# Performance work log

Measured on AMD Instinct MI355X. Metric: run time of the kernel, lower is better.

Reference implementation:

```python
import jax, jax.numpy as jnp
import numpy as np
import math

B_SZ, T_LEN, DIM = 1, 1024, 1024
D_STATE, EXPAND, NUM_SCALES, CONV_K = 16, 2, 3, 4
D_INNER = EXPAND * DIM
EPS_LOG = 1e-38
LN_EPS = 1e-5


def _causal_dwconv(x, w, b):
    # x: (B,T,D), w: (D,1,K) depthwise, b: (D,). torch Conv1d(pad=K-1)[:, :, :T] == left-pad K-1 (causal).
    y = jax.lax.conv_general_dilated(
        jnp.transpose(x, (0, 2, 1)), w, window_strides=(1,),
        padding=[(CONV_K - 1, 0)], dimension_numbers=('NCH', 'OIH', 'NCH'),
        feature_group_count=w.shape[0])
    return jnp.transpose(y, (0, 2, 1)) + b


def _ssm_core(x, cw, cb, xw, dtw, dtb, Dp):
    # x: (B,T,d_inner)
    xc = jax.nn.silu(_causal_dwconv(x, cw, cb))
    proj = xc @ xw.T                               # (B,T,2*d_state)
    B_ssm, C_ssm = proj[..., :D_STATE], proj[..., D_STATE:]
    dt = jax.nn.softplus(B_ssm @ dtw.T + dtb)      # (B,T,d_inner)
    dt = jax.nn.softplus(dt)                       # selective_scan applies softplus a second time (faithful)
    A = -jnp.arange(1, D_STATE + 1, dtype=xc.dtype)  # (d_state,) == -A_init row, same for every d_inner channel
    dA = jnp.exp(dt[..., None] * A)                # (B,T,d_inner,d_state)
    dBx = dt[..., None] * B_ssm[:, :, None, :] * xc[..., None]
    log_dA = jnp.log(jnp.clip(dA, EPS_LOG))
    log_dBx = jnp.log(jnp.clip(dBx, EPS_LOG))
    # parallel_scan_cpu: h = exp(cumsum(log_dA) + logcumsumexp(log_dBx - cumsum(log_dA)))
    a_star = jnp.cumsum(log_dA, axis=1)
    h = jnp.exp(a_star + jax.lax.cumlogsumexp(log_dBx - a_star, axis=1))
    return jnp.einsum('bts,btds->btd', C_ssm, h) + Dp * xc


def _downsample(x, stride):
    if stride == 1:
        return x
    Bb, T, D = x.shape
    Tt = (T // stride) * stride
    return x[:, :Tt].reshape(Bb, Tt // stride, stride, D).mean(2)


def _upsample(x, T_out):
    # F.interpolate(mode='linear', align_corners=False)
    T_in = x.shape[1]
    if T_in == T_out:
        return x
    scale = T_in / T_out
    pos = jnp.clip((jnp.arange(T_out, dtype=jnp.float32) + 0.5) * scale - 0.5, 0.0, T_in - 1)
    lo = jnp.floor(pos).astype(jnp.int32)
    hi = jnp.minimum(lo + 1, T_in - 1)
    w = (pos - lo.astype(pos.dtype))[None, :, None]
    return x[:, lo] * (1.0 - w) + x[:, hi] * w


def _forward(x, in_proj_w, conv_w, conv_b, xproj_w, dtproj_w, dtproj_b,
             D_param, scale_weights, gate_w1, gate_w2, out_proj_w, ln_g, ln_b):
    residual = x
    xz = x @ in_proj_w.T                           # (B,T,2*d_inner)
    x_in, gate = xz[..., :D_INNER], xz[..., D_INNER:]
    outs = []
    for s in range(NUM_SCALES):
        x_s = _downsample(x_in, 2 ** s)
        y_s = _ssm_core(x_s, conv_w[s], conv_b[s], xproj_w[s], dtproj_w[s], dtproj_b[s], D_param[s])
        outs.append(_upsample(y_s, x.shape[1]))
    w = jax.nn.softmax(scale_weights)
    fused = sum(w[s] * outs[s] for s in range(NUM_SCALES))
    ctx = sum(outs) / NUM_SCALES
    gate_ctx = jax.nn.sigmoid(jax.nn.silu(ctx @ gate_w1.T) @ gate_w2.T)
    out = (fused * gate_ctx) * jax.nn.silu(gate)
    out = out @ out_proj_w.T
    y = out + residual
    mu = y.mean(-1, keepdims=True)
    var = ((y - mu) ** 2).mean(-1, keepdims=True)
    return (y - mu) / jnp.sqrt(var + LN_EPS) * ln_g + ln_b


def setup_inputs() -> dict:
    key = jax.random.key(0)
    ks = jax.random.split(key, 12)
    g = lambda k, shp, s: (jax.random.normal(k, shp, jnp.float32) * s)
    return {
        'x': g(ks[0], (B_SZ, T_LEN, DIM), 1.0),
        'in_proj_w': g(ks[1], (2 * D_INNER, DIM), DIM ** -0.5),
        'conv_w': g(ks[2], (NUM_SCALES, D_INNER, 1, CONV_K), CONV_K ** -0.5),
        'conv_b': g(ks[3], (NUM_SCALES, D_INNER), 0.02),
        'xproj_w': g(ks[4], (NUM_SCALES, 2 * D_STATE, D_INNER), D_INNER ** -0.5),
        'dtproj_w': g(ks[5], (NUM_SCALES, D_INNER, D_STATE), D_STATE ** -0.5),
        'dtproj_b': jax.random.uniform(ks[6], (NUM_SCALES, D_INNER), jnp.float32,
                                       math.log(0.001), math.log(0.1)),
        'D_param': jnp.ones((NUM_SCALES, D_INNER), jnp.float32),
        'scale_weights': jnp.ones((NUM_SCALES,), jnp.float32) / NUM_SCALES,
        'gate_w1': g(ks[7], (D_INNER // 2, D_INNER), D_INNER ** -0.5),
        'gate_w2': g(ks[8], (D_INNER, D_INNER // 2), (D_INNER // 2) ** -0.5),
        'out_proj_w': g(ks[9], (DIM, D_INNER), D_INNER ** -0.5),
        'ln_g': jnp.ones((DIM,), jnp.float32),
        'ln_b': jnp.zeros((DIM,), jnp.float32),
    }


def reference(x, in_proj_w, conv_w, conv_b, xproj_w, dtproj_w, dtproj_b,
              D_param, scale_weights, gate_w1, gate_w2, out_proj_w, ln_g, ln_b):
    return _forward(x, in_proj_w, conv_w, conv_b, xproj_w, dtproj_w, dtproj_b,
                    D_param, scale_weights, gate_w1, gate_w2, out_proj_w, ln_g, ln_b)
```

## Files before the change

kernel.cpp:

```cpp
#include <hip/hip_runtime.h>

typedef unsigned short u16;
typedef float floatx4 __attribute__((ext_vector_type(4)));
typedef short shortx8 __attribute__((ext_vector_type(8)));

#define DIN 2048

__device__ __forceinline__ u16 f2bf(float f){
  unsigned u = __float_as_uint(f);
  u = (u + 0x7fffu + ((u>>16)&1u))>>16;
  return (u16)u;
}
__device__ __forceinline__ float sigf(float x){ return 1.f/(1.f+__expf(-x)); }
__device__ __forceinline__ float siluf(float x){ return x*sigf(x); }

#define OFF_WINP  0ull
#define OFF_WG1   8388608ull
#define OFF_WG2   12582912ull
#define OFF_WOP   16777216ull
#define OFF_XB    20971520ull
#define OFF_XIN   23068672ull
#define OFF_SGATE 31457280ull
#define OFF_X1    39845888ull
#define OFF_X2    44040192ull
#define OFF_XC0   46137344ull
#define OFF_XC1   54525952ull
#define OFF_XC2   58720256ull
#define OFF_FUSED 60817408ull
#define OFF_G3O   69206016ull
#define OFF_Y0    75497472ull
#define OFF_Y1    83886080ull
#define OFF_Y2    88080384ull
#define OFF_P0    90177536ull
#define OFF_P1    90308608ull
#define OFF_P2    90374144ull
#define OFF_CTXB  OFF_XC0
#define OFF_T1B   OFF_XC1
#define OFF_PS    OFF_Y0
#define OFF_HINIT OFF_XIN
#define OFF_T1A0  OFF_XIN
#define OFF_T1A1  OFF_X1
#define OFF_YPA0  OFF_Y1
#define OFF_YPA1  (OFF_XC0 + 4194304ull)
#define OFF_DT0   OFF_FUSED
#define OFF_DT1   OFF_G3O
#define OFF_DT2   (OFF_G3O + 4194304ull)

__device__ __forceinline__ void gld_lds16(const void* g, void* l){
  __builtin_amdgcn_global_load_lds((const __attribute__((address_space(1))) unsigned*)g,
                                   (__attribute__((address_space(3))) unsigned*)l, 16, 0, 0);
}

__global__ __launch_bounds__(256) void cvt_kernel(
    const float* __restrict__ s0, u16* __restrict__ d0,
    const float* __restrict__ s1, u16* __restrict__ d1,
    const float* __restrict__ s2, u16* __restrict__ d2,
    const float* __restrict__ s3, u16* __restrict__ d3,
    const float* __restrict__ s4, u16* __restrict__ d4)
{
  int i = (blockIdx.x*256 + threadIdx.x)*4;
  const float* s; u16* d;
  if      (i <  4194304){ s=s0; d=d0; }
  else if (i <  6291456){ s=s1; d=d1; i -=  4194304; }
  else if (i <  8388608){ s=s2; d=d2; i -=  6291456; }
  else if (i < 10485760){ s=s3; d=d3; i -=  8388608; }
  else                  { s=s4; d=d4; i -= 10485760; }
  const float4 v = *(const float4*)(s + i);
  ushort4 o; o.x = f2bf(v.x); o.y = f2bf(v.y); o.z = f2bf(v.z); o.w = f2bf(v.w);
  *(ushort4*)(d + i) = o;
}

template<int MODE, int BM>
__global__ __launch_bounds__(256) void gemm_bt(
    const u16* __restrict__ A, const u16* __restrict__ B,
    int N, int K, int Ks,
    float* __restrict__ out_f, float* __restrict__ out_f2, u16* __restrict__ out_b,
    const float* __restrict__ ex0f, const float* __restrict__ ex1f,
    float* __restrict__ ex0, float* __restrict__ ex1)
{
  constexpr int NI = BM/32;
  constexpr int IP = BM/64;
  __shared__ u16 smA[2][BM*32];
  __shared__ u16 smB[2][BM*32];
  const int tid  = threadIdx.x;
  const int m0   = blockIdx.y * BM;
  const int n0   = blockIdx.x * BM;
  const int wv   = tid >> 6;
  const int lane = tid & 63;
  const int mw   = (wv >> 1) * (BM/2);
  const int nw   = (wv & 1) * (BM/2);
  const int quad = lane >> 4;
  const int l16  = lane & 15;
  const int srow = tid >> 2;
  const int scol = (tid & 3) * 8;

  floatx4 acc[NI][NI];
#pragma unroll
  for (int i=0;i<NI;i++)
#pragma unroll
    for (int j=0;j<NI;j++) acc[i][j] = (floatx4)0.f;

  const int kStart = blockIdx.z * Ks;
  const int kEnd   = kStart + Ks;

  auto stage = [&](int buf, int k0){
#pragma unroll
    for (int p=0;p<IP;p++){
      gld_lds16(A + (size_t)(m0 + p*64 + srow)*K + k0 + scol, &smA[buf][p*2048 + wv*512]);
      gld_lds16(B + (size_t)(n0 + p*64 + srow)*K + k0 + scol, &smB[buf][p*2048 + wv*512]);
    }
  };

  stage(0, kStart);
  int cur = 0;
  for (int k0 = kStart; k0 < kEnd; k0 += 32) {
    __syncthreads();
    if (k0 + 32 < kEnd) stage(cur^1, k0+32);
    shortx8 af[NI], bfr[NI];
#pragma unroll
    for (int i=0;i<NI;i++){
      af[i]  = *(const shortx8*)&smA[cur][(mw + i*16 + l16)*32 + quad*8];
      bfr[i] = *(const shortx8*)&smB[cur][(nw + i*16 + l16)*32 + quad*8];
    }
#pragma unroll
    for (int i=0;i<NI;i++)
#pragma unroll
      for (int j=0;j<NI;j++)
        acc[i][j] = __builtin_amdgcn_mfma_f32_16x16x32_bf16(af[i], bfr[j], acc[i][j], 0, 0, 0);
    cur ^= 1;
  }

#pragma unroll
  for (int i=0;i<NI;i++){
    const int mb = m0 + mw + i*16 + quad*4;
#pragma unroll
    for (int j=0;j<NI;j++){
      const int n = n0 + nw + j*16 + l16;
      const floatx4 v4 = acc[i][j];
      if (MODE == 0){
        if (n < 2048){
#pragma unroll
          for (int r=0;r<4;r++) out_f[(size_t)(mb+r)*2048 + n] = v4[r];
          ex0[(size_t)(mb>>1)*2048 + n]       = 0.5f*(v4[0]+v4[1]);
          ex0[(size_t)((mb>>1)+1)*2048 + n]   = 0.5f*(v4[2]+v4[3]);
          ex1[(size_t)(mb>>2)*2048 + n]       = 0.25f*(v4[0]+v4[1]+v4[2]+v4[3]);
        } else {
#pragma unroll
          for (int r=0;r<4;r++) out_f2[(size_t)(mb+r)*2048 + (n-2048)] = siluf(v4[r]);
        }
      } else if (MODE == 2){
#pragma unroll
        for (int r=0;r<4;r++){
          const size_t idx = (size_t)(mb+r)*N + n;
          out_b[idx] = f2bf(sigf(v4[r]) * ex0f[idx] * ex1f[idx]);
        }
      } else {
        float* dst = blockIdx.z ? out_f2 : out_f;
#pragma unroll
        for (int r=0;r<4;r++) dst[(size_t)(mb+r)*N + n] = v4[r];
      }
    }
  }
}

__global__ __launch_bounds__(256) void g2_epi(const float* __restrict__ a,
    const float* __restrict__ b, u16* __restrict__ o){
  const int i = (blockIdx.x*256 + threadIdx.x)*4;
  const float4 va = *(const float4*)(a+i);
  const float4 vb = *(const float4*)(b+i);
  ushort4 r;
  r.x = f2bf(siluf(va.x+vb.x)); r.y = f2bf(siluf(va.y+vb.y));
  r.z = f2bf(siluf(va.z+vb.z)); r.w = f2bf(siluf(va.w+vb.w));
  *(ushort4*)(o+i) = r;
}

__global__ __launch_bounds__(256) void conv_kernel(const float* __restrict__ xin,
    const float* __restrict__ x1, const float* __restrict__ x2,
    const float* __restrict__ cw, const float* __restrict__ cb,
    float* __restrict__ xc0, float* __restrict__ xc1, float* __restrict__ xc2){
  const int idx = blockIdx.x*256 + threadIdx.x;
  const float* xs; float* xc; int s, local;
  if (idx < 1024*DIN)              { s=0; local=idx;             xs=xin; xc=xc0; }
  else if (idx < (1024+512)*DIN)   { s=1; local=idx-1024*DIN;    xs=x1;  xc=xc1; }
  else                             { s=2; local=idx-1536*DIN;    xs=x2;  xc=xc2; }
  const int t = local >> 11, d = local & 2047;
  const float* w = cw + ((size_t)(s*DIN) + d)*4;
  float acc = cb[s*DIN + d];
#pragma unroll
  for (int j=0;j<4;j++){
    const int tt = t - 3 + j;
    if (tt >= 0) acc += w[j] * xs[(size_t)tt*DIN + d];
  }
  xc[local] = siluf(acc);
}

__global__ __launch_bounds__(256) void xproj_kernel(const float* __restrict__ xc0,
    const float* __restrict__ xc1, const float* __restrict__ xc2,
    const float* __restrict__ xw,
    float* __restrict__ p0, float* __restrict__ p1, float* __restrict__ p2){
  __shared__ float srow[DIN];
  const int b = blockIdx.x;
  const float* xc; float* proj; int s, t;
  if (b < 1024)      { s=0; t=b;       xc=xc0; proj=p0; }
  else if (b < 1536) { s=1; t=b-1024;  xc=xc1; proj=p1; }
  else               { s=2; t=b-1536;  xc=xc2; proj=p2; }
  const float* xr = xc + (size_t)t*DIN;
  const int tid = threadIdx.x;
#pragma unroll
  for (int q=0;q<2;q++){
    const int k = (q*256 + tid)*4;
    *(float4*)&srow[k] = *(const float4*)&xr[k];
  }
  __syncthreads();
  const int i = tid >> 3;
  const int j = tid & 7;
  const float* w = xw + ((size_t)s*32 + i)*DIN;
  float acc = 0.f;
#pragma unroll 8
  for (int c=0;c<256;c++){
    const int k = j + 8*c;
    acc += srow[k]*w[k];
  }
  acc += __shfl_xor(acc,1); acc += __shfl_xor(acc,2); acc += __shfl_xor(acc,4);
  if (j == 0) proj[t*32 + i] = acc;
}

__global__ __launch_bounds__(128) void scan_p1(
    const float* __restrict__ xc0, const float* __restrict__ xc1, const float* __restrict__ xc2,
    const float* __restrict__ p0,  const float* __restrict__ p1,  const float* __restrict__ p2,
    const float* __restrict__ dtw, const float* __restrict__ dtb,
    float* __restrict__ dt0, float* __restrict__ dt1, float* __restrict__ dt2,
    float2* __restrict__ PS)
{
  __shared__ float sproj[32*32];
  int b = blockIdx.x;
  const float *xc, *proj; float* dto; int base, s;
  if (b < 512)      { xc=xc0; proj=p0; dto=dt0; base=0;  s=0; }
  else if (b < 768) { b-=512; xc=xc1; proj=p1; dto=dt1; base=32; s=1; }
  else              { b-=768; xc=xc2; proj=p2; dto=dt2; base=48; s=2; }
  const int chunk = b >> 4;
  const int tid   = threadIdx.x;
  const int d     = (b & 15)*128 + tid;
  const int t0    = chunk*32;
  {
    const int k = tid*8;
    *(float4*)&sproj[k]   = *(const float4*)&proj[t0*32 + k];
    *(float4*)&sproj[k+4] = *(const float4*)&proj[t0*32 + k + 4];
  }
  __syncthreads();

  float wreg[16];
  const float* wr = dtw + ((size_t)(s*DIN) + d)*16;
#pragma unroll
  for (int n=0;n<16;n++) wreg[n] = wr[n];
  const float bias = dtb[s*DIN + d];

  float H[16];
#pragma unroll
  for (int n=0;n<16;n++) H[n] = 0.f;
  float S = 0.f;
  const float* xcp = xc + (size_t)t0*DIN + d;
  float* dtp = dto + (size_t)t0*DIN + d;
  for (int tt=0; tt<32; tt++){
    const float xcv = xcp[(size_t)tt*DIN];
    const float* Bp = &sproj[tt*32];
    float z = bias;
#pragma unroll
    for (int n=0;n<16;n++) z += Bp[n]*wreg[n];
    z = fminf(z, 60.f);
    const float E     = __expf(z);
    const float denom = 2.f + E;
    const float e     = __builtin_amdgcn_rcpf(denom);
    const float dtv   = __logf(denom);
    dtp[(size_t)tt*DIN] = dtv;
    S += dtv;
    const float c = dtv*xcv;
    float ep = e;
#pragma unroll
    for (int n=0;n<16;n++){
      const float dA  = fmaxf(ep, 1e-38f);
      const float dBx = fmaxf(c*Bp[n], 1e-38f);
      H[n] = dA*H[n] + dBx;
      ep *= e;
    }
  }
  const float q = __expf(-S);
  float qp = q;
  float2* o = PS + ((size_t)(base+chunk)*2048 + d)*16;
#pragma unroll
  for (int n=0;n<16;n++){ float2 v; v.x = qp; v.y = H[n]; o[n] = v; qp *= q; }
}

__global__ __launch_bounds__(256) void scan_combine(const float2* __restrict__ PS,
                                                    float* __restrict__ Hinit){
  int id = blockIdx.x*256 + threadIdx.x;
  int base, C;
  if (id < 32768)      { base=0;  C=32; }
  else if (id < 65536) { id-=32768; base=32; C=16; }
  else                 { id-=65536; base=48; C=8;  }
  const size_t off = (size_t)base*32768 + id;
  const float2* ps = PS + off;
  float* hi = Hinit + off;
  float H = 0.f;
  for (int c=0;c<C;c++){
    hi[(size_t)c*32768] = H;
    const float2 v = ps[(size_t)c*32768];
    H = v.x*H + v.y;
  }
}

__global__ __launch_bounds__(128) void scan_p2(
    const float* __restrict__ xc0, const float* __restrict__ xc1, const float* __restrict__ xc2,
    const float* __restrict__ p0,  const float* __restrict__ p1,  const float* __restrict__ p2,
    const float* __restrict__ dt0, const float* __restrict__ dt1, const float* __restrict__ dt2,
    const float* __restrict__ Hinit, const float* __restrict__ Dp_all,
    float* __restrict__ y0, float* __restrict__ y1, float* __restrict__ y2)
{
  __shared__ float sproj[32*32];
  int b = blockIdx.x;
  const float *xc, *proj, *dti; float* y; int base, s;
  if (b < 512)      { xc=xc0; proj=p0; dti=dt0; y=y0; base=0;  s=0; }
  else if (b < 768) { b-=512; xc=xc1; proj=p1; dti=dt1; y=y1; base=32; s=1; }
  else              { b-=768; xc=xc2; proj=p2; dti=dt2; y=y2; base=48; s=2; }
  const int chunk = b >> 4;
  const int tid   = threadIdx.x;
  const int d     = (b & 15)*128 + tid;
  const int t0    = chunk*32;
  {
    const int k = tid*8;
    *(float4*)&sproj[k]   = *(const float4*)&proj[t0*32 + k];
    *(float4*)&sproj[k+4] = *(const float4*)&proj[t0*32 + k + 4];
  }
  __syncthreads();

  float H[16];
  const float* hi = Hinit + ((size_t)(base+chunk)*2048 + d)*16;
#pragma unroll
  for (int n=0;n<16;n++) H[n] = hi[n];
  const float Dv = Dp_all[s*DIN + d];
  const float* xcp = xc + (size_t)t0*DIN + d;
  const float* dtp = dti + (size_t)t0*DIN + d;
  float* yp = y + (size_t)t0*DIN + d;
  for (int tt=0; tt<32; tt++){
    const float xcv = xcp[(size_t)tt*DIN];
    const float dtv = dtp[(size_t)tt*DIN];
    const float* Bp = &sproj[tt*32];
    const float e = __expf(-dtv);
    const float c = dtv*xcv;
    float ep = e;
    float pacc = 0.f;
#pragma unroll
    for (int n=0;n<16;n++){
      const float dA  = fmaxf(ep, 1e-38f);
      const float dBx = fmaxf(c*Bp[n], 1e-38f);
      H[n] = dA*H[n] + dBx;
      pacc += Bp[16+n]*H[n];
      ep *= e;
    }
    yp[(size_t)tt*DIN] = pacc + Dv*xcv;
  }
}

__device__ __forceinline__ float ups_read(const float* __restrict__ ys, int Tin, int t, int d){
  const float scale = (float)Tin * (1.f/1024.f);
  float pos = ((float)t + 0.5f)*scale - 0.5f;
  pos = fminf(fmaxf(pos, 0.f), (float)(Tin-1));
  const int lo = (int)floorf(pos);
  const float w = pos - (float)lo;
  const int hi = min(lo+1, Tin-1);
  return ys[(size_t)lo*DIN + d]*(1.f-w) + ys[(size_t)hi*DIN + d]*w;
}

__global__ __launch_bounds__(256) void fuse_kernel(const float* __restrict__ y0,
    const float* __restrict__ y1, const float* __restrict__ y2,
    const float* __restrict__ sw, u16* __restrict__ ctxb, float* __restrict__ fused){
  const int idx = blockIdx.x*256 + threadIdx.x;
  const int t = idx >> 11, d = idx & 2047;
  const float w0r = sw[0], w1r = sw[1], w2r = sw[2];
  const float mx = fmaxf(w0r, fmaxf(w1r, w2r));
  float e0 = __expf(w0r-mx), e1 = __expf(w1r-mx), e2 = __expf(w2r-mx);
  const float inv = 1.f/(e0+e1+e2);
  e0 *= inv; e1 *= inv; e2 *= inv;
  const float o0 = y0[idx];
  const float o1 = ups_read(y1, 512, t, d);
  const float o2 = ups_read(y2, 256, t, d);
  fused[idx] = e0*o0 + e1*o1 + e2*o2;
  ctxb[idx]  = f2bf((o0+o1+o2)*(1.f/3.f));
}

__global__ __launch_bounds__(256) void ln_kernel(const float* __restrict__ ya,
    const float* __restrict__ yb, const float* __restrict__ xr,
    const float* __restrict__ g, const float* __restrict__ b, float* __restrict__ out){
  __shared__ float red[4];
  const int t = blockIdx.x;
  const size_t ro = (size_t)t*1024;
  float v[4];
  float s = 0.f;
#pragma unroll
  for (int i=0;i<4;i++){
    const int c = threadIdx.x + i*256;
    v[i] = ya[ro+c] + yb[ro+c] + xr[ro+c];
    s += v[i];
  }
  s += __shfl_xor(s,1); s += __shfl_xor(s,2); s += __shfl_xor(s,4);
  s += __shfl_xor(s,8); s += __shfl_xor(s,16); s += __shfl_xor(s,32);
  if ((threadIdx.x & 63) == 0) red[threadIdx.x>>6] = s;
  __syncthreads();
  const float mu = (red[0]+red[1]+red[2]+red[3]) * (1.f/1024.f);
  __syncthreads();
  float q = 0.f;
#pragma unroll
  for (int i=0;i<4;i++){ const float dd = v[i]-mu; q += dd*dd; }
  q += __shfl_xor(q,1); q += __shfl_xor(q,2); q += __shfl_xor(q,4);
  q += __shfl_xor(q,8); q += __shfl_xor(q,16); q += __shfl_xor(q,32);
  if ((threadIdx.x & 63) == 0) red[threadIdx.x>>6] = q;
  __syncthreads();
  const float rstd = rsqrtf((red[0]+red[1]+red[2]+red[3]) * (1.f/1024.f) + 1e-5f);
#pragma unroll
  for (int i=0;i<4;i++){
    const int c = threadIdx.x + i*256;
    out[ro + c] = (v[i]-mu)*rstd*g[c] + b[c];
  }
}

extern "C" void kernel_launch(void* const* d_in, const int* in_sizes, int n_in,
                              void* d_out, int out_size, void* d_ws, size_t ws_size,
                              hipStream_t stream) {
  const float* x     = (const float*)d_in[0];
  const float* inpw  = (const float*)d_in[1];
  const float* convw = (const float*)d_in[2];
  const float* convb = (const float*)d_in[3];
  const float* xpw   = (const float*)d_in[4];
  const float* dtw   = (const float*)d_in[5];
  const float* dtb   = (const float*)d_in[6];
  const float* Dp    = (const float*)d_in[7];
  const float* sw    = (const float*)d_in[8];
  const float* gw1   = (const float*)d_in[9];
  const float* gw2   = (const float*)d_in[10];
  const float* opw   = (const float*)d_in[11];
  const float* lng   = (const float*)d_in[12];
  const float* lnb   = (const float*)d_in[13];
  float* out = (float*)d_out;

  char* ws = (char*)d_ws;
  u16*    wInp  = (u16*)   (ws + OFF_WINP);
  u16*    wG1   = (u16*)   (ws + OFF_WG1);
  u16*    wG2   = (u16*)   (ws + OFF_WG2);
  u16*    wOp   = (u16*)   (ws + OFF_WOP);
  u16*    xb    = (u16*)   (ws + OFF_XB);
  float*  xin   = (float*) (ws + OFF_XIN);
  float*  sgate = (float*) (ws + OFF_SGATE);
  float*  x1    = (float*) (ws + OFF_X1);
  float*  x2    = (float*) (ws + OFF_X2);
  float*  xc0   = (float*) (ws + OFF_XC0);
  float*  xc1   = (float*) (ws + OFF_XC1);
  float*  xc2   = (float*) (ws + OFF_XC2);
  float*  dt0   = (float*) (ws + OFF_DT0);
  float*  dt1   = (float*) (ws + OFF_DT1);
  float*  dt2   = (float*) (ws + OFF_DT2);
  float*  y0    = (float*) (ws + OFF_Y0);
  float*  y1    = (float*) (ws + OFF_Y1);
  float*  y2    = (float*) (ws + OFF_Y2);
  float*  p0    = (float*) (ws + OFF_P0);
  float*  p1    = (float*) (ws + OFF_P1);
  float*  p2    = (float*) (ws + OFF_P2);
  float2* PS    = (float2*)(ws + OFF_PS);
  float*  Hinit = (float*) (ws + OFF_HINIT);
  u16*    ctxb  = (u16*)   (ws + OFF_CTXB);
  u16*    t1b   = (u16*)   (ws + OFF_T1B);
  float*  fused = (float*) (ws + OFF_FUSED);
  u16*    g3o   = (u16*)   (ws + OFF_G3O);
  float*  t1a0  = (float*) (ws + OFF_T1A0);
  float*  t1a1  = (float*) (ws + OFF_T1A1);
  float*  ypa0  = (float*) (ws + OFF_YPA0);
  float*  ypa1  = (float*) (ws + OFF_YPA1);

  cvt_kernel<<<11264, 256, 0, stream>>>(inpw, wInp, gw1, wG1, gw2, wG2, opw, wOp, x, xb);
  gemm_bt<0,64><<<dim3(64, 16, 1), 256, 0, stream>>>(xb, wInp, 4096, 1024, 1024,
                                                     xin, sgate, nullptr, nullptr, nullptr, x1, x2);
  conv_kernel<<<(1792*DIN)/256, 256, 0, stream>>>(xin, x1, x2, convw, convb, xc0, xc1, xc2);
  xproj_kernel<<<1792, 256, 0, stream>>>(xc0, xc1, xc2, xpw, p0, p1, p2);
  scan_p1<<<896, 128, 0, stream>>>(xc0, xc1, xc2, p0, p1, p2, dtw, dtb,
                                   dt0, dt1, dt2, PS);
  scan_combine<<<384, 256, 0, stream>>>(PS, Hinit);
  scan_p2<<<896, 128, 0, stream>>>(xc0, xc1, xc2, p0, p1, p2, dt0, dt1, dt2,
                                   Hinit, Dp, y0, y1, y2);
  fuse_kernel<<<(1024*DIN)/256, 256, 0, stream>>>(y0, y1, y2, sw, ctxb, fused);
  gemm_bt<4,64><<<dim3(16, 16, 2), 256, 0, stream>>>(ctxb, wG1, 1024, 2048, 1024,
                                                     t1a0, t1a1, nullptr, nullptr, nullptr, nullptr, nullptr);
  g2_epi<<<1024, 256, 0, stream>>>(t1a0, t1a1, t1b);
  gemm_bt<2,64><<<dim3(32, 16, 1), 256, 0, stream>>>(t1b, wG2, 2048, 1024, 1024,
                                                     nullptr, nullptr, g3o, fused, sgate, nullptr, nullptr);
  gemm_bt<4,64><<<dim3(16, 16, 2), 256, 0, stream>>>(g3o, wOp, 1024, 2048, 1024,
                                                     ypa0, ypa1, nullptr, nullptr, nullptr, nullptr, nullptr);
  ln_kernel<<<1024, 256, 0, stream>>>(ypa0, ypa1, x, lng, lnb, out);
}
```

Measured before the change: 302.9 us.

## Halve scan chunk length and pack scan state updates into float2 ops

The chunked selective scan now uses 16-step chunks instead of 32, which doubles the number of blocks in both scan passes and makes the sequential combine pass twice as long. The partial-state and initial-state buffers move to new dedicated workspace offsets because they grew. The inner state recurrences are also rewritten on float2 vectors, so the compiler can emit packed FP32 math, and the decay powers are computed two at a time. The aim is better occupancy and latency hiding in the scan kernels, paid for with more partial-state traffic and a longer serial combine.

```diff
diff --git a/kernel.cpp b/kernel.cpp
--- a/kernel.cpp
+++ b/kernel.cpp
@@ -1,6 +1,7 @@
 #include <hip/hip_runtime.h>
 
 typedef unsigned short u16;
+typedef float floatx2 __attribute__((ext_vector_type(2)));
 typedef float floatx4 __attribute__((ext_vector_type(4)));
 typedef short shortx8 __attribute__((ext_vector_type(8)));
 
@@ -13,6 +14,9 @@
 }
 __device__ __forceinline__ float sigf(float x){ return 1.f/(1.f+__expf(-x)); }
 __device__ __forceinline__ float siluf(float x){ return x*sigf(x); }
+__device__ __forceinline__ floatx2 max2(floatx2 a, floatx2 b){
+  floatx2 r; r.x = fmaxf(a.x, b.x); r.y = fmaxf(a.y, b.y); return r;
+}
 
 #define OFF_WINP  0ull
 #define OFF_WG1   8388608ull
@@ -34,10 +38,10 @@
 #define OFF_P0    90177536ull
 #define OFF_P1    90308608ull
 #define OFF_P2    90374144ull
+#define OFF_PS    92274688ull
+#define OFF_HINIT 121634816ull
 #define OFF_CTXB  OFF_XC0
 #define OFF_T1B   OFF_XC1
-#define OFF_PS    OFF_Y0
-#define OFF_HINIT OFF_XIN
 #define OFF_T1A0  OFF_XIN
 #define OFF_T1A1  OFF_X1
 #define OFF_YPA0  OFF_Y1
@@ -232,72 +236,78 @@
     float* __restrict__ dt0, float* __restrict__ dt1, float* __restrict__ dt2,
     float2* __restrict__ PS)
 {
-  __shared__ float sproj[32*32];
+  __shared__ float sproj[16*32];
   int b = blockIdx.x;
   const float *xc, *proj; float* dto; int base, s;
-  if (b < 512)      { xc=xc0; proj=p0; dto=dt0; base=0;  s=0; }
-  else if (b < 768) { b-=512; xc=xc1; proj=p1; dto=dt1; base=32; s=1; }
-  else              { b-=768; xc=xc2; proj=p2; dto=dt2; base=48; s=2; }
+  if (b < 1024)      { xc=xc0; proj=p0; dto=dt0; base=0;  s=0; }
+  else if (b < 1536) { b-=1024; xc=xc1; proj=p1; dto=dt1; base=64; s=1; }
+  else               { b-=1536; xc=xc2; proj=p2; dto=dt2; base=96; s=2; }
   const int chunk = b >> 4;
   const int tid   = threadIdx.x;
   const int d     = (b & 15)*128 + tid;
-  const int t0    = chunk*32;
+  const int t0    = chunk*16;
   {
-    const int k = tid*8;
-    *(float4*)&sproj[k]   = *(const float4*)&proj[t0*32 + k];
-    *(float4*)&sproj[k+4] = *(const float4*)&proj[t0*32 + k + 4];
+    const int k = tid*4;
+    *(float4*)&sproj[k] = *(const float4*)&proj[t0*32 + k];
   }
   __syncthreads();
 
-  float wreg[16];
-  const float* wr = dtw + ((size_t)(s*DIN) + d)*16;
-#pragma unroll
-  for (int n=0;n<16;n++) wreg[n] = wr[n];
+  floatx2 w2[8];
+  const floatx2* wr = (const floatx2*)(dtw + ((size_t)(s*DIN) + d)*16);
+#pragma unroll
+  for (int k=0;k<8;k++) w2[k] = wr[k];
   const float bias = dtb[s*DIN + d];
-
-  float H[16];
-#pragma unroll
-  for (int n=0;n<16;n++) H[n] = 0.f;
+  const floatx2 eps2 = {1e-38f, 1e-38f};
+
+  floatx2 H2[8];
+#pragma unroll
+  for (int k=0;k<8;k++) H2[k] = (floatx2)0.f;
   float S = 0.f;
   const float* xcp = xc + (size_t)t0*DIN + d;
   float* dtp = dto + (size_t)t0*DIN + d;
-  for (int tt=0; tt<32; tt++){
+  for (int tt=0; tt<16; tt++){
     const float xcv = xcp[(size_t)tt*DIN];
-    const float* Bp = &sproj[tt*32];
-    float z = bias;
-#pragma unroll
-    for (int n=0;n<16;n++) z += Bp[n]*wreg[n];
-    z = fminf(z, 60.f);
+    const floatx2* Bp2 = (const floatx2*)&sproj[tt*32];
+    floatx2 zz = (floatx2)0.f;
+#pragma unroll
+    for (int k=0;k<8;k++) zz += Bp2[k]*w2[k];
+    float z = fminf(zz.x + zz.y + bias, 60.f);
     const float E     = __expf(z);
     const float denom = 2.f + E;
     const float e     = __builtin_amdgcn_rcpf(denom);
     const float dtv   = __logf(denom);
     dtp[(size_t)tt*DIN] = dtv;
     S += dtv;
-    const float c = dtv*xcv;
-    float ep = e;
-#pragma unroll
-    for (int n=0;n<16;n++){
-      const float dA  = fmaxf(ep, 1e-38f);
-      const float dBx = fmaxf(c*Bp[n], 1e-38f);
-      H[n] = dA*H[n] + dBx;
-      ep *= e;
+    const floatx2 c2  = {dtv*xcv, dtv*xcv};
+    const floatx2 es  = {e*e, e*e};
+    floatx2 ep2 = {e, e*e};
+#pragma unroll
+    for (int k=0;k<8;k++){
+      const floatx2 dA  = max2(ep2, eps2);
+      const floatx2 dBx = max2(c2*Bp2[k], eps2);
+      H2[k] = dA*H2[k] + dBx;
+      ep2 *= es;
     }
   }
   const float q = __expf(-S);
-  float qp = q;
+  const floatx2 qs = {q*q, q*q};
+  floatx2 qp2 = {q, q*q};
   float2* o = PS + ((size_t)(base+chunk)*2048 + d)*16;
 #pragma unroll
-  for (int n=0;n<16;n++){ float2 v; v.x = qp; v.y = H[n]; o[n] = v; qp *= q; }
+  for (int k=0;k<8;k++){
+    float2 v0; v0.x = qp2.x; v0.y = H2[k].x; o[2*k]   = v0;
+    float2 v1; v1.x = qp2.y; v1.y = H2[k].y; o[2*k+1] = v1;
+    qp2 *= qs;
+  }
 }
 
 __global__ __launch_bounds__(256) void scan_combine(const float2* __restrict__ PS,
                                                     float* __restrict__ Hinit){
   int id = blockIdx.x*256 + threadIdx.x;
   int base, C;
-  if (id < 32768)      { base=0;  C=32; }
-  else if (id < 65536) { id-=32768; base=32; C=16; }
-  else                 { id-=65536; base=48; C=8;  }
+  if (id < 32768)      { base=0;  C=64; }
+  else if (id < 65536) { id-=32768; base=64; C=32; }
+  else                 { id-=65536; base=96; C=16; }
   const size_t off = (size_t)base*32768 + id;
   const float2* ps = PS + off;
   float* hi = Hinit + off;
@@ -316,48 +326,49 @@
     const float* __restrict__ Hinit, const float* __restrict__ Dp_all,
     float* __restrict__ y0, float* __restrict__ y1, float* __restrict__ y2)
 {
-  __shared__ float sproj[32*32];
+  __shared__ float sproj[16*32];
   int b = blockIdx.x;
   const float *xc, *proj, *dti; float* y; int base, s;
-  if (b < 512)      { xc=xc0; proj=p0; dti=dt0; y=y0; base=0;  s=0; }
-  else if (b < 768) { b-=512; xc=xc1; proj=p1; dti=dt1; y=y1; base=32; s=1; }
-  else              { b-=768; xc=xc2; proj=p2; dti=dt2; y=y2; base=48; s=2; }
+  if (b < 1024)      { xc=xc0; proj=p0; dti=dt0; y=y0; base=0;  s=0; }
+  else if (b < 1536) { b-=1024; xc=xc1; proj=p1; dti=dt1; y=y1; base=64; s=1; }
+  else               { b-=1536; xc=xc2; proj=p2; dti=dt2; y=y2; base=96; s=2; }
   const int chunk = b >> 4;
   const int tid   = threadIdx.x;
   const int d     = (b & 15)*128 + tid;
-  const int t0    = chunk*32;
+  const int t0    = chunk*16;
   {
-    const int k = tid*8;
-    *(float4*)&sproj[k]   = *(const float4*)&proj[t0*32 + k];
-    *(float4*)&sproj[k+4] = *(const float4*)&proj[t0*32 + k + 4];
+    const int k = tid*4;
+    *(float4*)&sproj[k] = *(const float4*)&proj[t0*32 + k];
   }
   __syncthreads();
 
-  float H[16];
-  const float* hi = Hinit + ((size_t)(base+chunk)*2048 + d)*16;
-#pragma unroll
-  for (int n=0;n<16;n++) H[n] = hi[n];
+  floatx2 H2[8];
+  const floatx2* hi = (const floatx2*)(Hinit + ((size_t)(base+chunk)*2048 + d)*16);
+#pragma unroll
+  for (int k=0;k<8;k++) H2[k] = hi[k];
   const float Dv = Dp_all[s*DIN + d];
+  const floatx2 eps2 = {1e-38f, 1e-38f};
   const float* xcp = xc + (size_t)t0*DIN + d;
   const float* dtp = dti + (size_t)t0*DIN + d;
   float* yp = y + (size_t)t0*DIN + d;
-  for (int tt=0; tt<32; tt++){
+  for (int tt=0; tt<16; tt++){
     const float xcv = xcp[(size_t)tt*DIN];
     const float dtv = dtp[(size_t)tt*DIN];
-    const float* Bp = &sproj[tt*32];
+    const floatx2* Bp2 = (const floatx2*)&sproj[tt*32];
     const float e = __expf(-dtv);
-    const float c = dtv*xcv;
-    float ep = e;
-    float pacc = 0.f;
-#pragma unroll
-    for (int n=0;n<16;n++){
-      const float dA  = fmaxf(ep, 1e-38f);
-      const float dBx = fmaxf(c*Bp[n], 1e-38f);
-      H[n] = dA*H[n] + dBx;
-      pacc += Bp[16+n]*H[n];
-      ep *= e;
+    const floatx2 c2 = {dtv*xcv, dtv*xcv};
+    const floatx2 es = {e*e, e*e};
+    floatx2 ep2 = {e, e*e};
+    floatx2 pacc2 = (floatx2)0.f;
+#pragma unroll
+    for (int k=0;k<8;k++){
+      const floatx2 dA  = max2(ep2, eps2);
+      const floatx2 dBx = max2(c2*Bp2[k], eps2);
+      H2[k] = dA*H2[k] + dBx;
+      pacc2 += Bp2[8+k]*H2[k];
+      ep2 *= es;
     }
-    yp[(size_t)tt*DIN] = pacc + Dv*xcv;
+    yp[(size_t)tt*DIN] = pacc2.x + pacc2.y + Dv*xcv;
   }
 }
 
@@ -480,11 +491,11 @@
                                                      xin, sgate, nullptr, nullptr, nullptr, x1, x2);
   conv_kernel<<<(1792*DIN)/256, 256, 0, stream>>>(xin, x1, x2, convw, convb, xc0, xc1, xc2);
   xproj_kernel<<<1792, 256, 0, stream>>>(xc0, xc1, xc2, xpw, p0, p1, p2);
-  scan_p1<<<896, 128, 0, stream>>>(xc0, xc1, xc2, p0, p1, p2, dtw, dtb,
-                                   dt0, dt1, dt2, PS);
+  scan_p1<<<1792, 128, 0, stream>>>(xc0, xc1, xc2, p0, p1, p2, dtw, dtb,
+                                    dt0, dt1, dt2, PS);
   scan_combine<<<384, 256, 0, stream>>>(PS, Hinit);
-  scan_p2<<<896, 128, 0, stream>>>(xc0, xc1, xc2, p0, p1, p2, dt0, dt1, dt2,
-                                   Hinit, Dp, y0, y1, y2);
+  scan_p2<<<1792, 128, 0, stream>>>(xc0, xc1, xc2, p0, p1, p2, dt0, dt1, dt2,
+                                    Hinit, Dp, y0, y1, y2);
   fuse_kernel<<<(1024*DIN)/256, 256, 0, stream>>>(y0, y1, y2, sw, ctxb, fused);
   gemm_bt<4,64><<<dim3(16, 16, 2), 256, 0, stream>>>(ctxb, wG1, 1024, 2048, 1024,
                                                      t1a0, t1a1, nullptr, nullptr, nullptr, nullptr, nullptr);
```

Measured after the change: 299.5 us. About the same (-1.1%).
